# Kernel optimization log

Measured on AMD Instinct MI355X. Metric: run time of the kernel, lower is better.

Reference implementation:

```python
import jax, jax.numpy as jnp
import numpy as np

N, F, H, R, DEG, K = 8192, 64, 128, 3, 32, 32
TEMP = 0.3          # config.edge_temperature
NEG_SLOPE = 0.2     # LeakyReLU slope
EPS_LN = 1e-5
W_THRESH = 1e-6


def setup_inputs() -> dict:
    key = jax.random.key(0)
    ks = jax.random.split(key, 16)
    E = N * DEG
    # each node has DEG outgoing edges so no softmax row is empty (-inf everywhere)
    src = jnp.repeat(jnp.arange(N), DEG)
    tgt = jax.random.randint(ks[0], (E,), 0, N)
    edge_index = jnp.stack([src, tgt]).astype(jnp.int64)
    x = jax.random.normal(ks[1], (N, F), jnp.float32)
    edge_attr = jax.random.normal(ks[2], (E, 3), jnp.float32)
    s = lambda k, sh: jax.random.normal(k, sh, jnp.float32) * 0.05
    D = 2 * F + 3  # edge_input_dim
    params = dict(
        Ws1=s(ks[3], (D, H)), bs1=jnp.zeros(H), ln_g=jnp.ones(H), ln_b=jnp.zeros(H),
        Ws2=s(ks[4], (H, 1)), bs2=jnp.zeros(1),
        Wp=s(ks[5], (D, H)), bp=jnp.zeros(H),
        Wr1=s(ks[6], (F, H)), br1=jnp.zeros(H), Wr2=s(ks[7], (H, R)), br2=jnp.zeros(R),
        Wg1=s(ks[8], (R, H, H // 2)), bg1=jnp.zeros((R, H // 2)),
        Wg2=s(ks[9], (R, H // 2, 1)), bg2=jnp.zeros((R, 1)),
        Wc1=s(ks[10], (F, H)), bc1=jnp.zeros(H), Wc2=s(ks[11], (H, 1)), bc2=jnp.zeros(1),
    )
    return {"x": x, "edge_index": edge_index, "edge_attr": edge_attr, **params}


def reference(x, edge_index, edge_attr,
              Ws1, bs1, ln_g, ln_b, Ws2, bs2, Wp, bp,
              Wr1, br1, Wr2, br2, Wg1, bg1, Wg2, bg2,
              Wc1, bc1, Wc2, bc2):
    src, tgt = edge_index[0], edge_index[1]
    num_nodes = x.shape[0]

    # regime encoder on global mean state
    gs = x.mean(axis=0)
    regime_probs = jax.nn.softmax(jax.nn.relu(gs @ Wr1 + br1) @ Wr2 + br2)  # [R]

    # contagion detector (scalar level)
    contagion_level = jax.nn.sigmoid(jax.nn.relu(x @ Wc1 + bc1) @ Wc2 + bc2).mean()

    # gather -> edge MLP scorer with LayerNorm + LeakyReLU
    edge_input = jnp.concatenate([x[src], x[tgt], edge_attr], axis=-1)  # [E, 2F+3]
    h = edge_input @ Ws1 + bs1
    mu = h.mean(-1, keepdims=True)
    var = h.var(-1, keepdims=True)
    h = (h - mu) * jax.lax.rsqrt(var + EPS_LN) * ln_g + ln_b
    h = jnp.where(h >= 0, h, NEG_SLOPE * h)
    edge_scores_raw = h @ Ws2 + bs2  # [E, 1]

    # regime gating
    edge_hidden = jax.nn.relu(edge_input @ Wp + bp)  # [E, H]
    g1 = jax.nn.relu(jnp.einsum('eh,rhm->erm', edge_hidden, Wg1) + bg1)
    gates = jax.nn.sigmoid(jnp.einsum('erm,rmo->ero', g1, Wg2) + bg2)[..., 0]  # [E, R]
    gate_combined = (gates * regime_probs).sum(-1, keepdims=True)  # [E, 1]

    amp = 1.0 + 0.5 * contagion_level
    edge_scores = (edge_scores_raw * gate_combined * amp)[:, 0]  # [E]

    # scatter into dense NxN, masked softmax per source row, top-k
    M = jnp.full((num_nodes, num_nodes), -jnp.inf, x.dtype).at[src, tgt].set(edge_scores)
    P = jax.nn.softmax(M / TEMP, axis=-1)  # [N, N]
    topk_values, topk_indices = jax.lax.top_k(P, K)  # [N, K]

    # in-device compaction equivalent: weights below threshold zeroed (dropped edges)
    new_edge_weights = jnp.where(topk_values > W_THRESH, topk_values, 0.0)  # [N, K]
    return new_edge_weights, topk_indices
```

## Files before the change

### kernel.cpp

```cpp
#include <hip/hip_runtime.h>
#include <hip/hip_bf16.h>
#include <math.h>

#define NN 8192
#define FF 64
#define HH 128
#define RR 3
#define DEG 32
#define KK 32
#define EE (NN*DEG)
#define DD 131
#define TEMP 0.3f
#define NEG_SLOPE 0.2f
#define EPS_LN 1e-5f
#define W_THRESH 1e-6f

typedef float v2f __attribute__((ext_vector_type(2)));
__device__ __forceinline__ float4 ld4(const float* p) { return *(const float4*)p; }
#define PKFMA(a, b, c) __builtin_elementwise_fma((a), (b), (c))
#define AIDX(a, j) a[((j)>>2)*2 + (((j)&3)>>1)][(j)&1]
#define GIDX(r, g) gaccv[r][(g)>>1][(g)&1]


__global__ __launch_bounds__(256) void setup_kernel(
    const float* __restrict__ x,
    const float* __restrict__ Ws1, const float* __restrict__ Wp,
    const float* __restrict__ Wc1, const float* __restrict__ bc1,
    const float* __restrict__ Wc2, const float* __restrict__ bc2,
    float* __restrict__ PA, float* __restrict__ hdr)
{
    __shared__ float spool[12608];
    int t = threadIdx.x;
    int bid = blockIdx.x;

    if (bid < 1024) {
        float* xs = spool;
        float* wl = spool + 2080;
        int which = bid & 1;
        int ch    = (bid >> 1) & 1;
        int n0    = (bid >> 2) * 32;
        const float* base = which ? Wp : Ws1;

        for (int i = t; i < 2048; i += 256)
            xs[(i >> 6) * 65 + (i & 63)] = x[n0 * 64 + i];
        for (int it = 0; it < 4; it++) {
            int flat = (t + it * 256) * 4;
            int r = flat >> 6, c = flat & 63;
            *(float4*)&wl[flat] = ld4(&base[r * 128 + ch * 64 + c]);
        }
        __syncthreads();

        int row = t >> 3, colg = t & 7;
        float acc[8];
        #pragma unroll
        for (int j = 0; j < 8; j++) acc[j] = 0.f;
        const float* xr = &xs[row * 65];
        for (int k = 0; k < 64; k++) {
            float a = xr[k];
            const float* wr = &wl[k * 64 + colg * 8];
            #pragma unroll
            for (int jj = 0; jj < 2; jj++) {
                float4 w = ld4(wr + 4 * jj);
                acc[4*jj+0] += a * w.x; acc[4*jj+1] += a * w.y;
                acc[4*jj+2] += a * w.z; acc[4*jj+3] += a * w.w;
            }
        }
        float* outp = PA + (size_t)which * (NN * 128) + (size_t)(n0 + row) * 128 + ch * 64 + colg * 8;
        #pragma unroll
        for (int j = 0; j < 8; j++) outp[j] = acc[j];
    } else {
        float* xs = spool;
        float* wl = spool + 4160;
        float* cs = spool + 12352;
        int n0 = (bid - 1024) * 64;

        for (int i = 0; i < 16; i++) {
            int flat = t + i * 256;
            int r = flat >> 6, c = flat & 63;
            xs[r * 65 + c] = x[(n0 + r) * 64 + c];
        }
        for (int i = 0; i < 8; i++) {
            int flat = (t + i * 256) * 4;
            *(float4*)&wl[flat] = ld4(&Wc1[flat]);
        }
        __syncthreads();

        {
            int col = t & 63, g = t >> 6;
            float ps = 0.f;
            for (int r = g * 16; r < g * 16 + 16; r++) ps += xs[r * 65 + col];
            cs[g * 64 + col] = ps;
        }
        __syncthreads();
        if (t < 64) {
            float v = cs[t] + cs[64 + t] + cs[128 + t] + cs[192 + t];
            atomicAdd(&hdr[8 + t], v);
        }

        int r = t >> 2, q = t & 3;
        float accl = 0.f;
        for (int hh = 0; hh < 32; hh++) {
            int h = hh * 4 + q;
            float s = bc1[h];
            for (int i = 0; i < 64; i++) s += xs[r * 65 + i] * wl[i * 128 + h];
            accl += fmaxf(s, 0.f) * Wc2[h];
        }
        accl += __shfl_xor(accl, 1);
        accl += __shfl_xor(accl, 2);
        if (q == 0) {
            float lvl = 1.f / (1.f + expf(-(accl + bc2[0])));
            atomicAdd(&hdr[0], lvl);
        }
    }
}

__global__ __launch_bounds__(128) void regime_kernel(
    const float* __restrict__ Wr1, const float* __restrict__ br1,
    const float* __restrict__ Wr2, const float* __restrict__ br2,
    float* __restrict__ hdr)
{
    __shared__ float gsl[64];
    __shared__ float t1[128];
    int t = threadIdx.x;
    if (t < 64) gsl[t] = hdr[8 + t] * (1.f / (float)NN);
    __syncthreads();
    float a = br1[t];
    for (int i = 0; i < 64; i++) a += gsl[i] * Wr1[i * 128 + t];
    t1[t] = fmaxf(a, 0.f);
    __syncthreads();
    if (t < 3) {
        float v = br2[t];
        for (int h = 0; h < 128; h++) v += t1[h] * Wr2[h * 3 + t];
        gsl[32 + t] = v;
    }
    __syncthreads();
    if (t == 0) {
        float v0 = gsl[32], v1 = gsl[33], v2 = gsl[34];
        float m = fmaxf(v0, fmaxf(v1, v2));
        float e0 = expf(v0 - m), e1 = expf(v1 - m), e2 = expf(v2 - m);
        float inv = 1.f / (e0 + e1 + e2);
        hdr[1] = e0 * inv; hdr[2] = e1 * inv; hdr[3] = e2 * inv;
        hdr[4] = 1.f + 0.5f * (hdr[0] * (1.f / (float)NN));
    }
}

#define EIB_S 76
__global__ __launch_bounds__(256) void edge_fused_kernel(
    const int* __restrict__ tgt_idx, const float* __restrict__ edge_attr,
    const float* __restrict__ x,
    const float* __restrict__ Ws1, const float* __restrict__ bs1,
    const float* __restrict__ ln_g, const float* __restrict__ ln_b,
    const float* __restrict__ Ws2, const float* __restrict__ bs2,
    const float* __restrict__ Wp, const float* __restrict__ bp,
    const float* __restrict__ Wg1, const float* __restrict__ bg1,
    const float* __restrict__ Wg2, const float* __restrict__ bg2,
    const float* __restrict__ PA1, const float* __restrict__ PA2,
    const float* __restrict__ hdr, float* __restrict__ scores)
{
    __shared__ float pool[8000];
    float* EIB   = pool;
    float* WPan  = pool + 4864;
    float* ehTh  = pool;
    float* WgPan = pool + 4352;
    float* Gbuf  = pool;
    float* rawS  = pool + 7936;

    int t = threadIdx.x;
    int e0 = blockIdx.x * 64;

    {
        int r = t >> 2, q = t & 3;
        int ge = e0 + r;
        int tg = tgt_idx[ge];
        #pragma unroll
        for (int i = 0; i < 4; i++) {
            int col = q * 16 + 4 * i;
            *(float4*)&EIB[r * EIB_S + col] = ld4(&x[tg * 64 + col]);
        }
        if (q == 0) {
            float4 v;
            v.x = edge_attr[(size_t)ge * 3 + 0];
            v.y = edge_attr[(size_t)ge * 3 + 1];
            v.z = edge_attr[(size_t)ge * 3 + 2];
            v.w = 0.f;
            *(float4*)&EIB[r * EIB_S + 64] = v;
        } else if (q == 1) {
            *(float4*)&EIB[r * EIB_S + 68] = make_float4(0.f, 0.f, 0.f, 0.f);
        } else if (q == 2) {
            *(float4*)&EIB[r * EIB_S + 72] = make_float4(0.f, 0.f, 0.f, 0.f);
        }
    }

    int spr0, spc0, sdst0, spr1, spc1, sdst1, spr2, spc2, sdst2;
    const float *ssrc0, *ssrc1, *ssrc2;
    {
        int fid, mat, loc;
        fid = t;            mat = (fid >= 384) ? 1 : 0; loc = fid - mat * 384;
        spr0 = loc >> 5; spc0 = (loc & 31) * 4; sdst0 = mat * 1536 + spr0 * 128 + spc0;
        ssrc0 = mat ? Wp : Ws1;
        fid = 256 + t;      mat = (fid >= 384) ? 1 : 0; loc = fid - mat * 384;
        spr1 = loc >> 5; spc1 = (loc & 31) * 4; sdst1 = mat * 1536 + spr1 * 128 + spc1;
        ssrc1 = mat ? Wp : Ws1;
        fid = 512 + t;      mat = (fid >= 384) ? 1 : 0; loc = fid - mat * 384;
        spr2 = loc >> 5; spc2 = (loc & 31) * 4; sdst2 = mat * 1536 + spr2 * 128 + spc2;
        ssrc2 = mat ? Wp : Ws1;
    }
    int gdst0, gdst1, gdst2, goff0, goff1, goff2;
    {
        int fid, rr, loc, pr, pc;
        fid = t;        rr = fid >> 8; loc = fid & 255; pr = loc >> 4; pc = (loc & 15) * 4;
        gdst0 = rr * 1024 + pr * 64 + pc; goff0 = rr * 8192 + pr * 64 + pc;
        fid = 256 + t;  rr = fid >> 8; loc = fid & 255; pr = loc >> 4; pc = (loc & 15) * 4;
        gdst1 = rr * 1024 + pr * 64 + pc; goff1 = rr * 8192 + pr * 64 + pc;
        fid = 512 + t;  rr = fid >> 8; loc = fid & 255; pr = loc >> 4; pc = (loc & 15) * 4;
        gdst2 = rr * 1024 + pr * 64 + pc; goff2 = rr * 8192 + pr * 64 + pc;
    }

    #define LOADP(pp, w0_, w1_, w2_)                                          \
      { int _pr0 = 64 + (pp) * 12 + spr0;                                     \
        int _pr1 = 64 + (pp) * 12 + spr1;                                     \
        int _pr2 = 64 + (pp) * 12 + spr2;                                     \
        w0_ = (_pr0 < 131) ? ld4(&ssrc0[_pr0 * 128 + spc0]) : make_float4(0.f,0.f,0.f,0.f); \
        w1_ = (_pr1 < 131) ? ld4(&ssrc1[_pr1 * 128 + spc1]) : make_float4(0.f,0.f,0.f,0.f); \
        w2_ = (_pr2 < 131) ? ld4(&ssrc2[_pr2 * 128 + spc2]) : make_float4(0.f,0.f,0.f,0.f); }

    #define LOADG(gi_, g0_, g1_, g2_)                                         \
      { g0_ = ld4(&Wg1[goff0 + (gi_) * 1024]);                                \
        g1_ = ld4(&Wg1[goff1 + (gi_) * 1024]);                                \
        g2_ = ld4(&Wg1[goff2 + (gi_) * 1024]); }

    int tcol = t & 7, trow = t >> 3;
    const float* EIr0 = &EIB[(2 * trow) * EIB_S];
    const float* EIr1 = EIr0 + EIB_S;
    int src = (e0 + 2 * trow) >> 5;

    v2f accs0[8], accs1[8], accp0[8], accp1[8];

    {
        const float* p1 = &PA1[(size_t)src * 128 + tcol * 4];
        const float* p2 = &PA2[(size_t)src * 128 + tcol * 4];
        #pragma unroll
        for (int jj = 0; jj < 4; jj++) {
            float4 v;
            v = ld4(p1 + jj * 32);
            v2f lo1 = { v.x, v.y }, hi1 = { v.z, v.w };
            accs0[jj*2] = lo1; accs0[jj*2+1] = hi1;
            accs1[jj*2] = lo1; accs1[jj*2+1] = hi1;
            v = ld4(p2 + jj * 32);
            v2f lo2 = { v.x, v.y }, hi2 = { v.z, v.w };
            accp0[jj*2] = lo2; accp0[jj*2+1] = hi2;
            accp1[jj*2] = lo2; accp1[jj*2+1] = hi2;
        }
    }

    float4 wra, wrb, wrc;
    LOADP(0, wra, wrb, wrc);
    for (int p = 0; p < 6; p++) {
        __syncthreads();
        *(float4*)&WPan[sdst0] = wra;
        *(float4*)&WPan[sdst1] = wrb;
        *(float4*)&WPan[sdst2] = wrc;
        if (p < 5) LOADP(p + 1, wra, wrb, wrc);
        __syncthreads();
        #pragma unroll
        for (int kk = 0; kk < 12; kk++) {
            int k = p * 12 + kk;
            float a0 = EIr0[k];
            float a1 = EIr1[k];
            v2f a0v = { a0, a0 }, a1v = { a1, a1 };
            const float* ws = &WPan[kk * 128 + tcol * 4];
            const float* wq = ws + 1536;
            #pragma unroll
            for (int jj = 0; jj < 4; jj++) {
                float4 w1 = ld4(ws + jj * 32);
                v2f w1a = { w1.x, w1.y }, w1b = { w1.z, w1.w };
                accs0[jj*2]   = PKFMA(a0v, w1a, accs0[jj*2]);
                accs0[jj*2+1] = PKFMA(a0v, w1b, accs0[jj*2+1]);
                accs1[jj*2]   = PKFMA(a1v, w1a, accs1[jj*2]);
                accs1[jj*2+1] = PKFMA(a1v, w1b, accs1[jj*2+1]);
                float4 w2 = ld4(wq + jj * 32);
                v2f w2a = { w2.x, w2.y }, w2b = { w2.z, w2.w };
                accp0[jj*2]   = PKFMA(a0v, w2a, accp0[jj*2]);
                accp0[jj*2+1] = PKFMA(a0v, w2b, accp0[jj*2+1]);
                accp1[jj*2]   = PKFMA(a1v, w2a, accp1[jj*2]);
                accp1[jj*2+1] = PKFMA(a1v, w2b, accp1[jj*2+1]);
            }
        }
    }

    float4 gra, grb, grc;
    LOADG(0, gra, grb, grc);

    {
        float s0 = 0.f, ss0 = 0.f, s1 = 0.f, ss1 = 0.f;
        #pragma unroll
        for (int j = 0; j < 16; j++) {
            int col = tcol * 4 + (j >> 2) * 32 + (j & 3);
            float b = bs1[col];
            float u0 = AIDX(accs0, j) + b;  AIDX(accs0, j) = u0;
            float u1 = AIDX(accs1, j) + b;  AIDX(accs1, j) = u1;
            s0 += u0; ss0 += u0 * u0;
            s1 += u1; ss1 += u1 * u1;
        }
        #pragma unroll
        for (int m = 1; m < 8; m <<= 1) {
            s0 += __shfl_xor(s0, m);  ss0 += __shfl_xor(ss0, m);
            s1 += __shfl_xor(s1, m);  ss1 += __shfl_xor(ss1, m);
        }
        float mu0 = s0 * (1.f / 128.f), mu1 = s1 * (1.f / 128.f);
        float var0 = ss0 * (1.f / 128.f) - mu0 * mu0;
        float var1 = ss1 * (1.f / 128.f) - mu1 * mu1;
        float inv0 = 1.f / sqrtf(var0 + EPS_LN);
        float inv1 = 1.f / sqrtf(var1 + EPS_LN);
        float d0 = 0.f, d1 = 0.f;
        #pragma unroll
        for (int j = 0; j < 16; j++) {
            int col = tcol * 4 + (j >> 2) * 32 + (j & 3);
            float g = ln_g[col], bb = ln_b[col], w2 = Ws2[col];
            float y0 = (AIDX(accs0, j) - mu0) * inv0 * g + bb;
            float y1 = (AIDX(accs1, j) - mu1) * inv1 * g + bb;
            y0 = (y0 >= 0.f) ? y0 : NEG_SLOPE * y0;
            y1 = (y1 >= 0.f) ? y1 : NEG_SLOPE * y1;
            d0 += y0 * w2; d1 += y1 * w2;
        }
        #pragma unroll
        for (int m = 1; m < 8; m <<= 1) {
            d0 += __shfl_xor(d0, m); d1 += __shfl_xor(d1, m);
        }
        if (tcol == 0) {
            rawS[2 * trow]     = d0 + bs2[0];
            rawS[2 * trow + 1] = d1 + bs2[0];
        }
    }

    int gtr = t >> 4, gtc = t & 15;
    int grow = t >> 2, gq = t & 3;

    v2f gaccv[3][8];
    #pragma unroll
    for (int rr = 0; rr < 3; rr++)
        #pragma unroll
        for (int j = 0; j < 8; j++) gaccv[rr][j] = (v2f){ 0.f, 0.f };

    for (int hf = 0; hf < 2; hf++) {
        __syncthreads();
        #pragma unroll
        for (int j2 = 0; j2 < 8; j2++) {
            int j = hf * 8 + j2;
            int col = tcol * 4 + (j >> 2) * 32 + (j & 3);
            int lc = col - hf * 64;
            float b = bp[col];
            ehTh[lc * 68 + 2 * trow]     = fmaxf(AIDX(accp0, j) + b, 0.f);
            ehTh[lc * 68 + 2 * trow + 1] = fmaxf(AIDX(accp1, j) + b, 0.f);
        }
        for (int p = 0; p < 4; p++) {
            __syncthreads();
            *(float4*)&WgPan[gdst0] = gra;
            *(float4*)&WgPan[gdst1] = grb;
            *(float4*)&WgPan[gdst2] = grc;
            {
                int gi = hf * 4 + p;
                if (gi < 7) LOADG(gi + 1, gra, grb, grc);
            }
            __syncthreads();
            #pragma unroll
            for (int kk = 0; kk < 16; kk++) {
                float4 av = ld4(&ehTh[(p * 16 + kk) * 68 + 4 * gtr]);
                v2f ax = { av.x, av.x }, ay = { av.y, av.y };
                v2f az = { av.z, av.z }, aw = { av.w, av.w };
                #pragma unroll
                for (int rr = 0; rr < 3; rr++) {
                    float4 bv = ld4(&WgPan[rr * 1024 + kk * 64 + 4 * gtc]);
                    v2f bva = { bv.x, bv.y }, bvb = { bv.z, bv.w };
                    gaccv[rr][0] = PKFMA(ax, bva, gaccv[rr][0]);
                    gaccv[rr][1] = PKFMA(ax, bvb, gaccv[rr][1]);
                    gaccv[rr][2] = PKFMA(ay, bva, gaccv[rr][2]);
                    gaccv[rr][3] = PKFMA(ay, bvb, gaccv[rr][3]);
                    gaccv[rr][4] = PKFMA(az, bva, gaccv[rr][4]);
                    gaccv[rr][5] = PKFMA(az, bvb, gaccv[rr][5]);
                    gaccv[rr][6] = PKFMA(aw, bva, gaccv[rr][6]);
                    gaccv[rr][7] = PKFMA(aw, bvb, gaccv[rr][7]);
                }
            }
        }
    }

    float gc = 0.f;
    for (int rr = 0; rr < 3; rr++) {
        __syncthreads();
        #pragma unroll
        for (int j = 0; j < 4; j++) {
            float b = bg1[rr * 64 + 4 * gtc + j];
            float4 g;
            g.x = fmaxf(GIDX(rr, 0  + j) + b, 0.f);
            g.y = fmaxf(GIDX(rr, 4  + j) + b, 0.f);
            g.z = fmaxf(GIDX(rr, 8  + j) + b, 0.f);
            g.w = fmaxf(GIDX(rr, 12 + j) + b, 0.f);
            *(float4*)&Gbuf[(4 * gtc + j) * 68 + 4 * gtr] = g;
        }
        __syncthreads();
        float pacc = 0.f;
        #pragma unroll
        for (int j = 0; j < 16; j++) {
            int m = gq * 4 + (j >> 2) * 16 + (j & 3);
            pacc += Gbuf[m * 68 + grow] * Wg2[rr * 64 + m];
        }
        pacc += __shfl_xor(pacc, 1);
        pacc += __shfl_xor(pacc, 2);
        float gate = 1.f / (1.f + expf(-(pacc + bg2[rr])));
        gc += gate * hdr[1 + rr];
    }
    if (gq == 0) scores[e0 + grow] = rawS[grow] * gc * hdr[4];
}

__global__ __launch_bounds__(64) void finalize_kernel(
    const int* __restrict__ tgt_idx, const float* __restrict__ scores,
    float* __restrict__ out_w, float* __restrict__ out_i)
{
    __shared__ int   tl[64];
    __shared__ float pl[64];
    int j = threadIdx.x;
    int half = j >> 5;
    int jl = j & 31;
    int hb = half * 32;
    int row = blockIdx.x * 2 + half;
    int   tg = tgt_idx[row * 32 + jl];
    float s  = scores[row * 32 + jl];
    tl[j] = tg;
    __syncthreads();

    bool alive = true;
    for (int j2 = jl + 1; j2 < 32; j2++)
        if (tl[hb + j2] == tg) { alive = false; break; }
    float z = alive ? s * (1.f / TEMP) : -INFINITY;
    float m = z;
    #pragma unroll
    for (int mm = 1; mm < 32; mm <<= 1) m = fmaxf(m, __shfl_xor(m, mm));
    float p = alive ? expf(z - m) : 0.f;
    float sum = p;
    #pragma unroll
    for (int mm = 1; mm < 32; mm <<= 1) sum += __shfl_xor(sum, mm);
    p = p / sum;
    pl[j] = alive ? p : -1.f;
    __syncthreads();

    int rank = 0, dcount = 0;
    for (int j2 = 0; j2 < 32; j2++) {
        float pj = pl[hb + j2];
        if (pj >= 0.f) {
            dcount++;
            if (alive) {
                if (pj > p || (pj == p && tl[hb + j2] < tg)) rank++;
            }
        }
    }
    if (alive) {
        out_w[row * 32 + rank] = (p > W_THRESH) ? p : 0.f;
        out_i[row * 32 + rank] = (float)tg;
    }
    if (jl == 0) {
        int c = 0;
        for (int slot = dcount; slot < 32; slot++) {
            for (;;) {
                bool found = false;
                for (int q = 0; q < 32; q++) if (tl[hb + q] == c) { found = true; break; }
                if (!found) break;
                c++;
            }
            out_w[row * 32 + slot] = 0.f;
            out_i[row * 32 + slot] = (float)c;
            c++;
        }
    }
}

extern "C" void kernel_launch(void* const* d_in, const int* in_sizes, int n_in,
                              void* d_out, int out_size, void* d_ws, size_t ws_size,
                              hipStream_t stream)
{
    const float* x          = (const float*)d_in[0];
    const int*   edge_index = (const int*)  d_in[1];
    const float* edge_attr  = (const float*)d_in[2];
    const float* Ws1 = (const float*)d_in[3];
    const float* bs1 = (const float*)d_in[4];
    const float* ln_g = (const float*)d_in[5];
    const float* ln_b = (const float*)d_in[6];
    const float* Ws2 = (const float*)d_in[7];
    const float* bs2 = (const float*)d_in[8];
    const float* Wp  = (const float*)d_in[9];
    const float* bp  = (const float*)d_in[10];
    const float* Wr1 = (const float*)d_in[11];
    const float* br1 = (const float*)d_in[12];
    const float* Wr2 = (const float*)d_in[13];
    const float* br2 = (const float*)d_in[14];
    const float* Wg1 = (const float*)d_in[15];
    const float* bg1 = (const float*)d_in[16];
    const float* Wg2 = (const float*)d_in[17];
    const float* bg2 = (const float*)d_in[18];
    const float* Wc1 = (const float*)d_in[19];
    const float* bc1 = (const float*)d_in[20];
    const float* Wc2 = (const float*)d_in[21];
    const float* bc2 = (const float*)d_in[22];

    float* hdr    = (float*)d_ws;
    float* scores = hdr + 128;
    float* tabs   = scores + EE;
    const int* tgt = edge_index + EE;

    hipMemsetAsync(d_ws, 0, 512, stream);
    setup_kernel<<<1152, 256, 0, stream>>>(x, Ws1, Wp, Wc1, bc1, Wc2, bc2, tabs, hdr);
    regime_kernel<<<1, 128, 0, stream>>>(Wr1, br1, Wr2, br2, hdr);
    edge_fused_kernel<<<EE / 64, 256, 0, stream>>>(
        tgt, edge_attr, x, Ws1, bs1, ln_g, ln_b, Ws2, bs2, Wp, bp,
        Wg1, bg1, Wg2, bg2, tabs, tabs + (size_t)NN * 128, hdr, scores);
    finalize_kernel<<<NN / 2, 64, 0, stream>>>(
        tgt, scores, (float*)d_out, (float*)d_out + NN * KK);
}
```

Baseline: 425.8 us.

## Retile edge GEMM to 4 edges x 8 cols per thread with transposed input

```diff
diff --git a/kernel.cpp b/kernel.cpp
--- a/kernel.cpp
+++ b/kernel.cpp
@@ -18,7 +18,6 @@
 typedef float v2f __attribute__((ext_vector_type(2)));
 __device__ __forceinline__ float4 ld4(const float* p) { return *(const float4*)p; }
 #define PKFMA(a, b, c) __builtin_elementwise_fma((a), (b), (c))
-#define AIDX(a, j) a[((j)>>2)*2 + (((j)&3)>>1)][(j)&1]
 #define GIDX(r, g) gaccv[r][(g)>>1][(g)&1]
 
 
@@ -144,7 +143,8 @@
     }
 }
 
-#define EIB_S 76
+#define EIBT_S 68
+#define HS_S 132
 __global__ __launch_bounds__(256) void edge_fused_kernel(
     const int* __restrict__ tgt_idx, const float* __restrict__ edge_attr,
     const float* __restrict__ x,
@@ -157,13 +157,14 @@
     const float* __restrict__ PA1, const float* __restrict__ PA2,
     const float* __restrict__ hdr, float* __restrict__ scores)
 {
-    __shared__ float pool[8000];
-    float* EIB   = pool;
-    float* WPan  = pool + 4864;
+    __shared__ float pool[8512];
+    float* WPan  = pool;
+    float* EIB_T = pool + 3072;
+    float* hS    = pool;
     float* ehTh  = pool;
     float* WgPan = pool + 4352;
     float* Gbuf  = pool;
-    float* rawS  = pool + 7936;
+    float* rawS  = pool + 8448;
 
     int t = threadIdx.x;
     int e0 = blockIdx.x * 64;
@@ -175,21 +176,19 @@
         #pragma unroll
         for (int i = 0; i < 4; i++) {
             int col = q * 16 + 4 * i;
-            *(float4*)&EIB[r * EIB_S + col] = ld4(&x[tg * 64 + col]);
+            float4 v = ld4(&x[tg * 64 + col]);
+            EIB_T[(col + 0) * EIBT_S + r] = v.x;
+            EIB_T[(col + 1) * EIBT_S + r] = v.y;
+            EIB_T[(col + 2) * EIBT_S + r] = v.z;
+            EIB_T[(col + 3) * EIBT_S + r] = v.w;
         }
         if (q == 0) {
-            float4 v;
-            v.x = edge_attr[(size_t)ge * 3 + 0];
-            v.y = edge_attr[(size_t)ge * 3 + 1];
-            v.z = edge_attr[(size_t)ge * 3 + 2];
-            v.w = 0.f;
-            *(float4*)&EIB[r * EIB_S + 64] = v;
-        } else if (q == 1) {
-            *(float4*)&EIB[r * EIB_S + 68] = make_float4(0.f, 0.f, 0.f, 0.f);
-        } else if (q == 2) {
-            *(float4*)&EIB[r * EIB_S + 72] = make_float4(0.f, 0.f, 0.f, 0.f);
-        }
-    }
+            EIB_T[64 * EIBT_S + r] = edge_attr[(size_t)ge * 3 + 0];
+            EIB_T[65 * EIBT_S + r] = edge_attr[(size_t)ge * 3 + 1];
+            EIB_T[66 * EIBT_S + r] = edge_attr[(size_t)ge * 3 + 2];
+        }
+    }
+    if (t < 320) EIB_T[(67 + (t >> 6)) * EIBT_S + (t & 63)] = 0.f;
 
     int spr0, spc0, sdst0, spr1, spc1, sdst1, spr2, spc2, sdst2;
     const float *ssrc0, *ssrc1, *ssrc2;
@@ -229,27 +228,22 @@
         g1_ = ld4(&Wg1[goff1 + (gi_) * 1024]);                                \
         g2_ = ld4(&Wg1[goff2 + (gi_) * 1024]); }
 
-    int tcol = t & 7, trow = t >> 3;
-    const float* EIr0 = &EIB[(2 * trow) * EIB_S];
-    const float* EIr1 = EIr0 + EIB_S;
-    int src = (e0 + 2 * trow) >> 5;
-
-    v2f accs0[8], accs1[8], accp0[8], accp1[8];
-
+    int ed = t >> 4, cd = t & 15;
+    int eb = ed * 4, cb = cd * 8;
+    int srcg = (e0 + eb) >> 5;
+
+    v2f aS[4][4], aP[4][4];
     {
-        const float* p1 = &PA1[(size_t)src * 128 + tcol * 4];
-        const float* p2 = &PA2[(size_t)src * 128 + tcol * 4];
-        #pragma unroll
-        for (int jj = 0; jj < 4; jj++) {
-            float4 v;
-            v = ld4(p1 + jj * 32);
-            v2f lo1 = { v.x, v.y }, hi1 = { v.z, v.w };
-            accs0[jj*2] = lo1; accs0[jj*2+1] = hi1;
-            accs1[jj*2] = lo1; accs1[jj*2+1] = hi1;
-            v = ld4(p2 + jj * 32);
-            v2f lo2 = { v.x, v.y }, hi2 = { v.z, v.w };
-            accp0[jj*2] = lo2; accp0[jj*2+1] = hi2;
-            accp1[jj*2] = lo2; accp1[jj*2+1] = hi2;
+        const float* p1 = &PA1[(size_t)srcg * 128 + cb];
+        const float* p2 = &PA2[(size_t)srcg * 128 + cb];
+        float4 v0 = ld4(p1), v1 = ld4(p1 + 4);
+        float4 u0 = ld4(p2), u1 = ld4(p2 + 4);
+        #pragma unroll
+        for (int e = 0; e < 4; e++) {
+            aS[e][0] = (v2f){ v0.x, v0.y }; aS[e][1] = (v2f){ v0.z, v0.w };
+            aS[e][2] = (v2f){ v1.x, v1.y }; aS[e][3] = (v2f){ v1.z, v1.w };
+            aP[e][0] = (v2f){ u0.x, u0.y }; aP[e][1] = (v2f){ u0.z, u0.w };
+            aP[e][2] = (v2f){ u1.x, u1.y }; aP[e][3] = (v2f){ u1.z, u1.w };
         }
     }
 
@@ -265,40 +259,61 @@
         #pragma unroll
         for (int kk = 0; kk < 12; kk++) {
             int k = p * 12 + kk;
-            float a0 = EIr0[k];
-            float a1 = EIr1[k];
-            v2f a0v = { a0, a0 }, a1v = { a1, a1 };
-            const float* ws = &WPan[kk * 128 + tcol * 4];
+            float4 av = ld4(&EIB_T[k * EIBT_S + eb]);
+            const float* ws = &WPan[kk * 128 + cb];
             const float* wq = ws + 1536;
+            float4 w1 = ld4(ws), w2 = ld4(ws + 4);
+            float4 q1 = ld4(wq), q2 = ld4(wq + 4);
+            v2f w1a = { w1.x, w1.y }, w1b = { w1.z, w1.w };
+            v2f w1c = { w2.x, w2.y }, w1d = { w2.z, w2.w };
+            v2f q1a = { q1.x, q1.y }, q1b = { q1.z, q1.w };
+            v2f q1c = { q2.x, q2.y }, q1d = { q2.z, q2.w };
+            float ae[4] = { av.x, av.y, av.z, av.w };
             #pragma unroll
-            for (int jj = 0; jj < 4; jj++) {
-                float4 w1 = ld4(ws + jj * 32);
-                v2f w1a = { w1.x, w1.y }, w1b = { w1.z, w1.w };
-                accs0[jj*2]   = PKFMA(a0v, w1a, accs0[jj*2]);
-                accs0[jj*2+1] = PKFMA(a0v, w1b, accs0[jj*2+1]);
-                accs1[jj*2]   = PKFMA(a1v, w1a, accs1[jj*2]);
-                accs1[jj*2+1] = PKFMA(a1v, w1b, accs1[jj*2+1]);
-                float4 w2 = ld4(wq + jj * 32);
-                v2f w2a = { w2.x, w2.y }, w2b = { w2.z, w2.w };
-                accp0[jj*2]   = PKFMA(a0v, w2a, accp0[jj*2]);
-                accp0[jj*2+1] = PKFMA(a0v, w2b, accp0[jj*2+1]);
-                accp1[jj*2]   = PKFMA(a1v, w2a, accp1[jj*2]);
-                accp1[jj*2+1] = PKFMA(a1v, w2b, accp1[jj*2+1]);
-            }
-        }
-    }
-
+            for (int e = 0; e < 4; e++) {
+                v2f aa = { ae[e], ae[e] };
+                aS[e][0] = PKFMA(aa, w1a, aS[e][0]);
+                aS[e][1] = PKFMA(aa, w1b, aS[e][1]);
+                aS[e][2] = PKFMA(aa, w1c, aS[e][2]);
+                aS[e][3] = PKFMA(aa, w1d, aS[e][3]);
+                aP[e][0] = PKFMA(aa, q1a, aP[e][0]);
+                aP[e][1] = PKFMA(aa, q1b, aP[e][1]);
+                aP[e][2] = PKFMA(aa, q1c, aP[e][2]);
+                aP[e][3] = PKFMA(aa, q1d, aP[e][3]);
+            }
+        }
+    }
+
+    __syncthreads();
+    #pragma unroll
+    for (int e = 0; e < 4; e++) {
+        float4 g0, g1;
+        g0.x = aS[e][0][0]; g0.y = aS[e][0][1]; g0.z = aS[e][1][0]; g0.w = aS[e][1][1];
+        g1.x = aS[e][2][0]; g1.y = aS[e][2][1]; g1.z = aS[e][3][0]; g1.w = aS[e][3][1];
+        *(float4*)&hS[(eb + e) * HS_S + cb]     = g0;
+        *(float4*)&hS[(eb + e) * HS_S + cb + 4] = g1;
+    }
     float4 gra, grb, grc;
     LOADG(0, gra, grb, grc);
-
+    __syncthreads();
+
+    int tcol = t & 7, trow = t >> 3;
     {
+        float h0[16], h1[16];
+        #pragma unroll
+        for (int jj = 0; jj < 4; jj++) {
+            float4 a0 = ld4(&hS[(2 * trow) * HS_S + tcol * 4 + jj * 32]);
+            float4 a1 = ld4(&hS[(2 * trow + 1) * HS_S + tcol * 4 + jj * 32]);
+            h0[jj*4+0] = a0.x; h0[jj*4+1] = a0.y; h0[jj*4+2] = a0.z; h0[jj*4+3] = a0.w;
+            h1[jj*4+0] = a1.x; h1[jj*4+1] = a1.y; h1[jj*4+2] = a1.z; h1[jj*4+3] = a1.w;
+        }
         float s0 = 0.f, ss0 = 0.f, s1 = 0.f, ss1 = 0.f;
         #pragma unroll
         for (int j = 0; j < 16; j++) {
             int col = tcol * 4 + (j >> 2) * 32 + (j & 3);
             float b = bs1[col];
-            float u0 = AIDX(accs0, j) + b;  AIDX(accs0, j) = u0;
-            float u1 = AIDX(accs1, j) + b;  AIDX(accs1, j) = u1;
+            float u0 = h0[j] + b;  h0[j] = u0;
+            float u1 = h1[j] + b;  h1[j] = u1;
             s0 += u0; ss0 += u0 * u0;
             s1 += u1; ss1 += u1 * u1;
         }
@@ -317,8 +332,8 @@
         for (int j = 0; j < 16; j++) {
             int col = tcol * 4 + (j >> 2) * 32 + (j & 3);
             float g = ln_g[col], bb = ln_b[col], w2 = Ws2[col];
-            float y0 = (AIDX(accs0, j) - mu0) * inv0 * g + bb;
-            float y1 = (AIDX(accs1, j) - mu1) * inv1 * g + bb;
+            float y0 = (h0[j] - mu0) * inv0 * g + bb;
+            float y1 = (h1[j] - mu1) * inv1 * g + bb;
             y0 = (y0 >= 0.f) ? y0 : NEG_SLOPE * y0;
             y1 = (y1 >= 0.f) ? y1 : NEG_SLOPE * y1;
             d0 += y0 * w2; d1 += y1 * w2;
@@ -344,14 +359,20 @@
 
     for (int hf = 0; hf < 2; hf++) {
         __syncthreads();
-        #pragma unroll
-        for (int j2 = 0; j2 < 8; j2++) {
-            int j = hf * 8 + j2;
-            int col = tcol * 4 + (j >> 2) * 32 + (j & 3);
-            int lc = col - hf * 64;
-            float b = bp[col];
-            ehTh[lc * 68 + 2 * trow]     = fmaxf(AIDX(accp0, j) + b, 0.f);
-            ehTh[lc * 68 + 2 * trow + 1] = fmaxf(AIDX(accp1, j) + b, 0.f);
+        if ((cd >> 3) == hf) {
+            int lcb = cb - hf * 64;
+            #pragma unroll
+            for (int jo = 0; jo < 8; jo++) {
+                int j = (jo + cd) & 7;
+                int c = cb + j;
+                float b = bp[c];
+                float4 g;
+                g.x = fmaxf(aP[0][j >> 1][j & 1] + b, 0.f);
+                g.y = fmaxf(aP[1][j >> 1][j & 1] + b, 0.f);
+                g.z = fmaxf(aP[2][j >> 1][j & 1] + b, 0.f);
+                g.w = fmaxf(aP[3][j >> 1][j & 1] + b, 0.f);
+                *(float4*)&ehTh[(lcb + j) * 68 + eb] = g;
+            }
         }
         for (int p = 0; p < 4; p++) {
             __syncthreads();
```

After: 504.8 us. 18.5% more time.
